# Optimization experiments

Measured on AMD Instinct MI355X. Metric: run time of the kernel, lower is better.

## Reference

```python
import jax, jax.numpy as jnp
import numpy as np

E = 8        # num_experts
K = 2        # num_experts_per_tok
H = 1024     # hidden_dim
F = 2816     # intermediate_dim
R = 256      # shared-core rank
B, S = 2, 1024


def setup_inputs() -> dict:
    key = jax.random.key(0)
    ks = jax.random.split(key, 12)
    inp = {
        "hidden_states": jax.random.normal(ks[0], (B, S, H), jnp.float32),
        "gate_w": jax.random.normal(ks[1], (H, E), jnp.float32) / np.sqrt(H),
        # gate_proj: hidden -> intermediate, factored W_e = Ug[e] @ Cg @ Vg[e]
        "Ug": jax.random.normal(ks[2], (E, H, R), jnp.float32) / np.sqrt(H),
        "Cg": jax.random.normal(ks[3], (R, R), jnp.float32) / np.sqrt(R),
        "Vg": jax.random.normal(ks[4], (E, R, F), jnp.float32) / np.sqrt(R),
        # up_proj: hidden -> intermediate
        "Uu": jax.random.normal(ks[5], (E, H, R), jnp.float32) / np.sqrt(H),
        "Cu": jax.random.normal(ks[6], (R, R), jnp.float32) / np.sqrt(R),
        "Vu": jax.random.normal(ks[7], (E, R, F), jnp.float32) / np.sqrt(R),
        # down_proj: intermediate -> hidden
        "Ud": jax.random.normal(ks[8], (E, F, R), jnp.float32) / np.sqrt(F),
        "Cd": jax.random.normal(ks[9], (R, R), jnp.float32) / np.sqrt(R),
        "Vd": jax.random.normal(ks[10], (E, R, H), jnp.float32) / np.sqrt(R),
    }
    return inp


def _moe_forward(x, gate_w, Ug, Cg, Vg, Uu, Cu, Vu, Ud, Cd, Vd):
    b, s, h = x.shape
    xf = x.reshape(-1, h)                       # [T, H]
    T = xf.shape[0]
    logits = xf @ gate_w                        # [T, E]
    probs = jax.nn.softmax(logits, axis=-1)
    w, idx = jax.lax.top_k(probs, K)            # [T, K]
    w = w / jnp.sum(w, axis=-1, keepdims=True)
    # dense combine weights: combine[t, e] = sum of renormalized routing
    # weights over top-k slots routed to expert e (scatter-add in torch code)
    combine = jnp.zeros((T, E), xf.dtype).at[jnp.arange(T)[:, None], idx].add(w)
    out = jnp.zeros_like(xf)
    for e in range(E):  # fixed small expert count
        g = (xf @ Ug[e]) @ Cg @ Vg[e]           # [T, F]
        u = (xf @ Uu[e]) @ Cu @ Vu[e]           # [T, F]
        a = jax.nn.silu(g) * u
        y = (a @ Ud[e]) @ Cd @ Vd[e]            # [T, H]
        out = out + combine[:, e:e + 1] * y
    return out.reshape(b, s, h)


def reference(hidden_states, gate_w, Ug, Cg, Vg, Uu, Cu, Vu, Ud, Cd, Vd):
    return _moe_forward(hidden_states, gate_w, Ug, Cg, Vg, Uu, Cu, Vu, Ud, Cd, Vd)
```

## Files before the change

kernel.cpp:

```cpp
#include <hip/hip_runtime.h>
#include <math.h>

constexpr int cE = 8;
constexpr int cH = 1024;
constexpr int cF = 2816;
constexpr int cR = 256;
constexpr int cT = 2048;
constexpr int ROWS = cT * 2;
constexpr int LDA = 40;

using short8  = __attribute__((ext_vector_type(8))) short;
using float4v = __attribute__((ext_vector_type(4))) float;
#define MFMA16 __builtin_amdgcn_mfma_f32_16x16x32_bf16

__device__ __forceinline__ unsigned short f2bf(float f) {
  union { float f; unsigned u; } v; v.f = f;
  unsigned r = v.u + 0x7fffu + ((v.u >> 16) & 1u);
  return (unsigned short)(r >> 16);
}
__device__ __forceinline__ float bf2f(unsigned short s) {
  union { unsigned u; float f; } v; v.u = (unsigned)s << 16; return v.f;
}

__device__ __forceinline__ void store_bf8(unsigned short* dst, float4 a, float4 b) {
  union { unsigned short u[8]; uint4 v; } t;
  t.u[0] = f2bf(a.x); t.u[1] = f2bf(a.y); t.u[2] = f2bf(a.z); t.u[3] = f2bf(a.w);
  t.u[4] = f2bf(b.x); t.u[5] = f2bf(b.y); t.u[6] = f2bf(b.z); t.u[7] = f2bf(b.w);
  *reinterpret_cast<uint4*>(dst) = t.v;
}

__device__ __forceinline__ void gld16(const unsigned short* g, unsigned short* l) {
  __builtin_amdgcn_global_load_lds(
      (const __attribute__((address_space(1))) void*)g,
      (__attribute__((address_space(3))) void*)l, 16, 0, 0);
}

__global__ __launch_bounds__(256) void k_gating(
    const float* __restrict__ x, const float* __restrict__ gw,
    unsigned short* __restrict__ xb, int* __restrict__ et,
    float* __restrict__ wt)
{
  const int tid = threadIdx.x;
  const int wid = tid >> 6, lane = tid & 63;
  const int t = blockIdx.x * 4 + wid;
  const float* xr = x + (long)t * cH + lane * 16;
  float4 v0 = *reinterpret_cast<const float4*>(xr);
  float4 v1 = *reinterpret_cast<const float4*>(xr + 4);
  float4 v2 = *reinterpret_cast<const float4*>(xr + 8);
  float4 v3 = *reinterpret_cast<const float4*>(xr + 12);
  store_bf8(xb + (long)t * cH + lane * 16, v0, v1);
  store_bf8(xb + (long)t * cH + lane * 16 + 8, v2, v3);
  float xv[16];
  *reinterpret_cast<float4*>(&xv[0])  = v0;
  *reinterpret_cast<float4*>(&xv[4])  = v1;
  *reinterpret_cast<float4*>(&xv[8])  = v2;
  *reinterpret_cast<float4*>(&xv[12]) = v3;
  const float* g = gw + (long)lane * 16 * cE;
  float l[cE];
#pragma unroll
  for (int e = 0; e < cE; ++e) l[e] = 0.f;
#pragma unroll
  for (int i = 0; i < 16; ++i) {
    float4 ga = *reinterpret_cast<const float4*>(g + i * cE);
    float4 gb = *reinterpret_cast<const float4*>(g + i * cE + 4);
    float xi = xv[i];
    l[0] += xi * ga.x; l[1] += xi * ga.y; l[2] += xi * ga.z; l[3] += xi * ga.w;
    l[4] += xi * gb.x; l[5] += xi * gb.y; l[6] += xi * gb.z; l[7] += xi * gb.w;
  }
#pragma unroll
  for (int m = 1; m < 64; m <<= 1)
#pragma unroll
    for (int e = 0; e < cE; ++e)
      l[e] += __shfl_xor(l[e], m, 64);
  if (lane == 0) {
    int i0 = 0; float m0 = l[0];
#pragma unroll
    for (int e = 1; e < cE; ++e) if (l[e] > m0) { m0 = l[e]; i0 = e; }
    int i1 = -1; float m1 = -1e30f;
#pragma unroll
    for (int e = 0; e < cE; ++e) if (e != i0 && l[e] > m1) { m1 = l[e]; i1 = e; }
    float w0 = 1.f / (1.f + expf(m1 - m0));
    et[t * 2 + 0] = i0;  et[t * 2 + 1] = i1;
    wt[t * 2 + 0] = w0;  wt[t * 2 + 1] = 1.f - w0;
  }
}

__global__ __launch_bounds__(256) void k_lists(
    const int* __restrict__ et, int* __restrict__ rowmap,
    int* __restrict__ tok, int* __restrict__ cnt, int* __restrict__ off)
{
  __shared__ int c[cE], p[cE], o[cE];
  const int tid = threadIdx.x;
  if (tid < cE) { c[tid] = 0; p[tid] = 0; }
  __syncthreads();
  for (int i = tid; i < ROWS; i += 256) atomicAdd(&c[et[i]], 1);
  __syncthreads();
  if (tid == 0) {
    int s = 0;
    for (int e = 0; e < cE; ++e) { o[e] = s; s += c[e]; }
  }
  __syncthreads();
  for (int i = tid; i < ROWS; i += 256) {
    int e = et[i];
    int slot = atomicAdd(&p[e], 1);
    int cr = o[e] + slot;
    rowmap[i] = cr;
    tok[cr] = i >> 1;
  }
  if (tid < cE) { cnt[tid] = c[tid]; off[tid] = o[tid]; }
}

__device__ __forceinline__ void tconv_tile(
    const float* __restrict__ in, unsigned short* __restrict__ out,
    int P, int Q, int e, int bx, int by, int tid, float (*tile)[33])
{
  const long es = (long)P * Q;
  in += e * es; out += e * es;
  const int c0 = bx * 32, r0 = by * 32;
  const int r = tid >> 3, c4 = (tid & 7) * 4;
  float4 v = *reinterpret_cast<const float4*>(in + (long)(r0 + r) * Q + c0 + c4);
  tile[r][c4 + 0] = v.x; tile[r][c4 + 1] = v.y;
  tile[r][c4 + 2] = v.z; tile[r][c4 + 3] = v.w;
  __syncthreads();
  const int cc = tid >> 3, rr4 = (tid & 7) * 4;
  ushort4 o;
  o.x = f2bf(tile[rr4 + 0][cc]);
  o.y = f2bf(tile[rr4 + 1][cc]);
  o.z = f2bf(tile[rr4 + 2][cc]);
  o.w = f2bf(tile[rr4 + 3][cc]);
  *reinterpret_cast<ushort4*>(out + (long)(c0 + cc) * P + r0 + rr4) = o;
}

constexpr int TCONV_BLOCKS = 19072;
__global__ __launch_bounds__(256) void k_tconv_all(
    const float* __restrict__ Cg, unsigned short* __restrict__ CgT,
    const float* __restrict__ Cu, unsigned short* __restrict__ CuT,
    const float* __restrict__ Vd, unsigned short* __restrict__ VdT,
    const float* __restrict__ Vg, unsigned short* __restrict__ vgT,
    const float* __restrict__ Vu, unsigned short* __restrict__ vuT,
    const float* __restrict__ Ud, unsigned short* __restrict__ udT)
{
  __shared__ float tile[32][33];
  int b = blockIdx.x;
  const float* in; unsigned short* out; int P, Q;
  if (b < 64)         { in = Cg; out = CgT; P = 256;  Q = 256;  }
  else if (b < 128)   { b -= 64;    in = Cu; out = CuT; P = 256;  Q = 256;  }
  else if (b < 2176)  { b -= 128;   in = Vd; out = VdT; P = 256;  Q = 1024; }
  else if (b < 7808)  { b -= 2176;  in = Vg; out = vgT; P = 256;  Q = 2816; }
  else if (b < 13440) { b -= 7808;  in = Vu; out = vuT; P = 256;  Q = 2816; }
  else                { b -= 13440; in = Ud; out = udT; P = 2816; Q = 256;  }
  const int tpe = (P / 32) * (Q / 32);
  const int e = b / tpe, rem = b % tpe;
  const int bx = rem % (Q / 32), by = rem / (Q / 32);
  tconv_tile(in, out, P, Q, e, bx, by, threadIdx.x, tile);
}

__device__ __forceinline__ void foldm_body(
    const unsigned short* __restrict__ A, const float* __restrict__ B,
    unsigned short* __restrict__ D, int ldd, int m0, int n0, int tid,
    unsigned short* As, unsigned short* Bs)
{
  const int sr = tid >> 2, sk = (tid & 3) * 8;
  const unsigned short* a0 = A + (long)(m0 + sr) * 256 + sk;
  const unsigned short* a1 = a0 + (long)64 * 256;
  const float* br = B + (long)(n0 + sr) * 256 + sk;
  uint4 rA0, rA1; float4 rB0, rB1;
  auto load_slice = [&](int k0) {
    rA0 = *reinterpret_cast<const uint4*>(a0 + k0);
    rA1 = *reinterpret_cast<const uint4*>(a1 + k0);
    rB0 = *reinterpret_cast<const float4*>(br + k0);
    rB1 = *reinterpret_cast<const float4*>(br + k0 + 4);
  };
  load_slice(0);
  const int wid = tid >> 6, lane = tid & 63;
  const int wm = (wid >> 1) * 64, wn = (wid & 1) * 32;
  const int fr = lane & 15, fq = lane >> 4;
  float4v zf = {0.f, 0.f, 0.f, 0.f};
  float4v acc[4][2];
#pragma unroll
  for (int i = 0; i < 4; ++i) { acc[i][0] = zf; acc[i][1] = zf; }
  for (int k0 = 0; k0 < 256; k0 += 32) {
    *reinterpret_cast<uint4*>(&As[sr * LDA + sk]) = rA0;
    *reinterpret_cast<uint4*>(&As[(sr + 64) * LDA + sk]) = rA1;
    store_bf8(&Bs[sr * LDA + sk], rB0, rB1);
    if (k0 + 32 < 256) load_slice(k0 + 32);
    __syncthreads();
    short8 af[4], bf[2];
#pragma unroll
    for (int mi = 0; mi < 4; ++mi)
      af[mi] = *reinterpret_cast<const short8*>(&As[(wm + mi * 16 + fr) * LDA + fq * 8]);
#pragma unroll
    for (int nj = 0; nj < 2; ++nj)
      bf[nj] = *reinterpret_cast<const short8*>(&Bs[(wn + nj * 16 + fr) * LDA + fq * 8]);
#pragma unroll
    for (int mi = 0; mi < 4; ++mi)
#pragma unroll
      for (int nj = 0; nj < 2; ++nj)
        acc[mi][nj] = MFMA16(af[mi], bf[nj], acc[mi][nj], 0, 0, 0);
    __syncthreads();
  }
#pragma unroll
  for (int mi = 0; mi < 4; ++mi)
#pragma unroll
    for (int r = 0; r < 4; ++r) {
      int m = m0 + wm + mi * 16 + fq * 4 + r;
#pragma unroll
      for (int nj = 0; nj < 2; ++nj)
        D[(long)m * ldd + n0 + wn + nj * 16 + fr] = f2bf(acc[mi][nj][r]);
    }
}

__global__ __launch_bounds__(256, 2) void k_foldm(
    const unsigned short* __restrict__ A, long sA,
    const float* __restrict__ B, long sB,
    unsigned short* __restrict__ D, long sD, int ldd)
{
  __shared__ __align__(16) unsigned short As[128 * LDA], Bs[64 * LDA];
  const int e = blockIdx.z;
  foldm_body(A + e * sA, B + e * sB, D + e * sD, ldd,
             blockIdx.y * 128, blockIdx.x * 64, threadIdx.x, As, Bs);
}

__global__ __launch_bounds__(256, 2) void k_foldm2(
    const unsigned short* __restrict__ A0, const unsigned short* __restrict__ A1,
    const float* __restrict__ B0, const float* __restrict__ B1,
    unsigned short* __restrict__ D)
{
  __shared__ __align__(16) unsigned short As[128 * LDA], Bs[64 * LDA];
  const int z = blockIdx.z, sel = z >> 3, e = z & 7;
  const unsigned short* A = sel ? A1 : A0;
  const float* B = (sel ? B1 : B0) + (long)e * cH * cR;
  unsigned short* Dp = D + (long)e * 512 * 1024 + (long)sel * 256 * 1024;
  foldm_body(A, B, Dp, cH, blockIdx.y * 128, blockIdx.x * 64, threadIdx.x, As, Bs);
}

__global__ __launch_bounds__(256, 2) void k_t1c(
    const unsigned short* __restrict__ xb, const unsigned short* __restrict__ b1t,
    unsigned short* __restrict__ t1, const int* __restrict__ tok,
    const int* __restrict__ cnt, const int* __restrict__ off)
{
  __shared__ __align__(16) unsigned short As[128 * 64], Bs[64 * 64];
  const int e = blockIdx.z, c = cnt[e], o = off[e];
  const int m0 = blockIdx.y * 128;
  if (m0 >= c) return;
  const int n0 = blockIdx.x * 64;
  const int tid = threadIdx.x;
  const int wid = tid >> 6, lane = tid & 63;
  const int sr8 = lane >> 3, sc = (lane & 7) * 8;
  const unsigned short* gA[4];
#pragma unroll
  for (int j = 0; j < 4; ++j) {
    int row = min(m0 + wid * 32 + j * 8 + sr8, c - 1);
    gA[j] = xb + (long)tok[o + row] * cH + sc;
  }
  const unsigned short* gB = b1t + (long)e * 512 * 1024 +
      (long)(n0 + wid * 16 + sr8) * 1024 + sc;
  unsigned short* lA = As + wid * 32 * 64;
  unsigned short* lB = Bs + wid * 16 * 64;
  const int wm = (wid >> 1) * 64, wn = (wid & 1) * 32;
  const int fr = lane & 15, fq = lane >> 4;
  float4v zf = {0.f, 0.f, 0.f, 0.f};
  float4v acc[4][2];
#pragma unroll
  for (int i = 0; i < 4; ++i) { acc[i][0] = zf; acc[i][1] = zf; }
  for (int k0 = 0; k0 < cH; k0 += 64) {
#pragma unroll
    for (int j = 0; j < 4; ++j) gld16(gA[j] + k0, lA + j * 8 * 64);
    gld16(gB + k0, lB);
    gld16(gB + (long)8 * 1024 + k0, lB + 8 * 64);
    __syncthreads();
#pragma unroll
    for (int ks = 0; ks < 2; ++ks) {
      short8 af[4], bf[2];
#pragma unroll
      for (int mi = 0; mi < 4; ++mi)
        af[mi] = *reinterpret_cast<const short8*>(
            &As[(wm + mi * 16 + fr) * 64 + ks * 32 + fq * 8]);
#pragma unroll
      for (int nj = 0; nj < 2; ++nj)
        bf[nj] = *reinterpret_cast<const short8*>(
            &Bs[(wn + nj * 16 + fr) * 64 + ks * 32 + fq * 8]);
#pragma unroll
      for (int mi = 0; mi < 4; ++mi)
#pragma unroll
        for (int nj = 0; nj < 2; ++nj)
          acc[mi][nj] = MFMA16(af[mi], bf[nj], acc[mi][nj], 0, 0, 0);
    }
    __syncthreads();
  }
#pragma unroll
  for (int mi = 0; mi < 4; ++mi)
#pragma unroll
    for (int r = 0; r < 4; ++r) {
      int row = m0 + wm + mi * 16 + fq * 4 + r;
      if (row < c) {
#pragma unroll
        for (int nj = 0; nj < 2; ++nj)
          t1[(long)(o + row) * 512 + n0 + wn + nj * 16 + fr] = f2bf(acc[mi][nj][r]);
      }
    }
}

__global__ __launch_bounds__(256, 2) void k_act(
    const unsigned short* __restrict__ t1,
    const unsigned short* __restrict__ vgT, const unsigned short* __restrict__ vuT,
    unsigned short* __restrict__ a, const int* __restrict__ cnt,
    const int* __restrict__ off)
{
  __shared__ __align__(16) unsigned short Ag[128 * 32], Au[128 * 32];
  __shared__ __align__(16) unsigned short Bg[64 * 32],  Bu[64 * 32];
  const int e = blockIdx.z, c = cnt[e], o = off[e];
  const int m0 = blockIdx.y * 128;
  if (m0 >= c) return;
  const int n0 = blockIdx.x * 64;
  const int tid = threadIdx.x;
  const int wid = tid >> 6, lane = tid & 63;
  const int sr16 = lane >> 2, sc = (lane & 3) * 8;
  const int ra0 = o + min(m0 + wid * 32 + sr16, c - 1);
  const int ra1 = o + min(m0 + wid * 32 + 16 + sr16, c - 1);
  const unsigned short* gAg0 = t1 + (long)ra0 * 512 + sc;
  const unsigned short* gAg1 = t1 + (long)ra1 * 512 + sc;
  const unsigned short* gBg = vgT + (long)e * cF * 256 + (long)(n0 + wid * 16 + sr16) * 256 + sc;
  const unsigned short* gBu = vuT + (long)e * cF * 256 + (long)(n0 + wid * 16 + sr16) * 256 + sc;
  unsigned short* lAg = Ag + wid * 32 * 32;
  unsigned short* lAu = Au + wid * 32 * 32;
  unsigned short* lBg = Bg + wid * 16 * 32;
  unsigned short* lBu = Bu + wid * 16 * 32;
  const int wm = (wid >> 1) * 64, wn = (wid & 1) * 32;
  const int fr = lane & 15, fq = lane >> 4;
  float4v zf = {0.f, 0.f, 0.f, 0.f};
  float4v accg[4][2], accu[4][2];
#pragma unroll
  for (int i = 0; i < 4; ++i) { accg[i][0] = zf; accg[i][1] = zf; accu[i][0] = zf; accu[i][1] = zf; }
  for (int k0 = 0; k0 < 256; k0 += 32) {
    gld16(gAg0 + k0, lAg);
    gld16(gAg1 + k0, lAg + 16 * 32);
    gld16(gAg0 + 256 + k0, lAu);
    gld16(gAg1 + 256 + k0, lAu + 16 * 32);
    gld16(gBg + k0, lBg);
    gld16(gBu + k0, lBu);
    __syncthreads();
    short8 ag[4], au[4], bg[2], bu[2];
#pragma unroll
    for (int mi = 0; mi < 4; ++mi) {
      ag[mi] = *reinterpret_cast<const short8*>(&Ag[(wm + mi * 16 + fr) * 32 + fq * 8]);
      au[mi] = *reinterpret_cast<const short8*>(&Au[(wm + mi * 16 + fr) * 32 + fq * 8]);
    }
#pragma unroll
    for (int nj = 0; nj < 2; ++nj) {
      bg[nj] = *reinterpret_cast<const short8*>(&Bg[(wn + nj * 16 + fr) * 32 + fq * 8]);
      bu[nj] = *reinterpret_cast<const short8*>(&Bu[(wn + nj * 16 + fr) * 32 + fq * 8]);
    }
#pragma unroll
    for (int mi = 0; mi < 4; ++mi)
#pragma unroll
      for (int nj = 0; nj < 2; ++nj) {
        accg[mi][nj] = MFMA16(ag[mi], bg[nj], accg[mi][nj], 0, 0, 0);
        accu[mi][nj] = MFMA16(au[mi], bu[nj], accu[mi][nj], 0, 0, 0);
      }
    __syncthreads();
  }
#pragma unroll
  for (int mi = 0; mi < 4; ++mi)
#pragma unroll
    for (int r = 0; r < 4; ++r) {
      int row = m0 + wm + mi * 16 + fq * 4 + r;
      if (row < c) {
#pragma unroll
        for (int nj = 0; nj < 2; ++nj) {
          float g = accg[mi][nj][r];
          float u = accu[mi][nj][r];
          float s = g / (1.f + expf(-g)) * u;
          a[(long)(o + row) * cF + n0 + wn + nj * 16 + fr] = f2bf(s);
        }
      }
    }
}

__global__ __launch_bounds__(256) void k_t3(
    const unsigned short* __restrict__ a, const unsigned short* __restrict__ udT,
    float* __restrict__ t3p, const int* __restrict__ cnt,
    const int* __restrict__ off)
{
  __shared__ __align__(16) unsigned short As[64 * 64], Bs[64 * 64];
  const int e = blockIdx.z, c = cnt[e], o = off[e];
  const int m0 = blockIdx.y * 64;
  if (m0 >= c) return;
  const int n0 = (blockIdx.x & 3) * 64;
  const int ksp = blockIdx.x >> 2;
  const int kbase = ksp * 704;
  const int tid = threadIdx.x;
  const int wid = tid >> 6, lane = tid & 63;
  const int sr8 = lane >> 3, sc = (lane & 7) * 8;
  const int ra0 = o + min(m0 + wid * 16 + sr8, c - 1);
  const int ra1 = o + min(m0 + wid * 16 + 8 + sr8, c - 1);
  const unsigned short* gA0 = a + (long)ra0 * cF + kbase + sc;
  const unsigned short* gA1 = a + (long)ra1 * cF + kbase + sc;
  const unsigned short* gB  = udT + (long)e * 256 * cF + (long)(n0 + wid * 16 + sr8) * cF + kbase + sc;
  unsigned short* lA = As + wid * 16 * 64;
  unsigned short* lB = Bs + wid * 16 * 64;
  const int wm = (wid >> 1) * 32, wn = (wid & 1) * 32;
  const int fr = lane & 15, fq = lane >> 4;
  float4v zf = {0.f, 0.f, 0.f, 0.f};
  float4v acc[2][2] = {{zf, zf}, {zf, zf}};
  for (int k0 = 0; k0 < 704; k0 += 64) {
    gld16(gA0 + k0, lA);
    gld16(gA1 + k0, lA + 8 * 64);
    gld16(gB + k0, lB);
    gld16(gB + (long)8 * cF + k0, lB + 8 * 64);
    __syncthreads();
#pragma unroll
    for (int ks = 0; ks < 2; ++ks) {
      short8 af[2], bf[2];
#pragma unroll
      for (int mi = 0; mi < 2; ++mi)
        af[mi] = *reinterpret_cast<const short8*>(
            &As[(wm + mi * 16 + fr) * 64 + ks * 32 + fq * 8]);
#pragma unroll
      for (int nj = 0; nj < 2; ++nj)
        bf[nj] = *reinterpret_cast<const short8*>(
            &Bs[(wn + nj * 16 + fr) * 64 + ks * 32 + fq * 8]);
#pragma unroll
      for (int mi = 0; mi < 2; ++mi)
#pragma unroll
        for (int nj = 0; nj < 2; ++nj)
          acc[mi][nj] = MFMA16(af[mi], bf[nj], acc[mi][nj], 0, 0, 0);
    }
    __syncthreads();
  }
  float* dstbase = t3p + (long)ksp * ROWS * 256;
#pragma unroll
  for (int mi = 0; mi < 2; ++mi)
#pragma unroll
    for (int r = 0; r < 4; ++r) {
      int row = m0 + wm + mi * 16 + fq * 4 + r;
      if (row < c) {
        float* dst = dstbase + (long)(o + row) * 256 + n0 + wn;
#pragma unroll
        for (int nj = 0; nj < 2; ++nj)
          dst[nj * 16 + fr] = acc[mi][nj][r];
      }
    }
}

__global__ __launch_bounds__(256) void k_red(
    const float* __restrict__ t3p, unsigned short* __restrict__ t3b)
{
  const long psz = (long)ROWS * 256;
  long i = ((long)blockIdx.x * 256 + threadIdx.x) * 8;
  float4 s0 = *reinterpret_cast<const float4*>(t3p + i);
  float4 s1 = *reinterpret_cast<const float4*>(t3p + i + 4);
#pragma unroll
  for (int q = 1; q < 4; ++q) {
    float4 a0 = *reinterpret_cast<const float4*>(t3p + q * psz + i);
    float4 a1 = *reinterpret_cast<const float4*>(t3p + q * psz + i + 4);
    s0.x += a0.x; s0.y += a0.y; s0.z += a0.z; s0.w += a0.w;
    s1.x += a1.x; s1.y += a1.y; s1.z += a1.z; s1.w += a1.w;
  }
  store_bf8(t3b + i, s0, s1);
}

__global__ __launch_bounds__(256, 2) void k_y(
    const unsigned short* __restrict__ t3b, const unsigned short* __restrict__ vd2t,
    unsigned short* __restrict__ y, const int* __restrict__ cnt,
    const int* __restrict__ off)
{
  __shared__ __align__(16) unsigned short As[128 * 32], Bs[64 * 32];
  const int e = blockIdx.z, c = cnt[e], o = off[e];
  const int m0 = blockIdx.y * 128;
  if (m0 >= c) return;
  const int n0 = blockIdx.x * 64;
  const int tid = threadIdx.x;
  const int wid = tid >> 6, lane = tid & 63;
  const int sr16 = lane >> 2, sc = (lane & 3) * 8;
  const int ra0 = o + min(m0 + wid * 32 + sr16, c - 1);
  const int ra1 = o + min(m0 + wid * 32 + 16 + sr16, c - 1);
  const unsigned short* gA0 = t3b + (long)ra0 * 256 + sc;
  const unsigned short* gA1 = t3b + (long)ra1 * 256 + sc;
  const unsigned short* gB  = vd2t + (long)e * cH * 256 + (long)(n0 + wid * 16 + sr16) * 256 + sc;
  unsigned short* lA = As + wid * 32 * 32;
  unsigned short* lB = Bs + wid * 16 * 32;
  const int wm = (wid >> 1) * 64, wn = (wid & 1) * 32;
  const int fr = lane & 15, fq = lane >> 4;
  float4v zf = {0.f, 0.f, 0.f, 0.f};
  float4v acc[4][2];
#pragma unroll
  for (int i = 0; i < 4; ++i) { acc[i][0] = zf; acc[i][1] = zf; }
  for (int k0 = 0; k0 < 256; k0 += 32) {
    gld16(gA0 + k0, lA);
    gld16(gA1 + k0, lA + 16 * 32);
    gld16(gB + k0, lB);
    __syncthreads();
    short8 af[4], bf[2];
#pragma unroll
    for (int mi = 0; mi < 4; ++mi)
      af[mi] = *reinterpret_cast<const short8*>(&As[(wm + mi * 16 + fr) * 32 + fq * 8]);
#pragma unroll
    for (int nj = 0; nj < 2; ++nj)
      bf[nj] = *reinterpret_cast<const short8*>(&Bs[(wn + nj * 16 + fr) * 32 + fq * 8]);
#pragma unroll
    for (int mi = 0; mi < 4; ++mi)
#pragma unroll
      for (int nj = 0; nj < 2; ++nj)
        acc[mi][nj] = MFMA16(af[mi], bf[nj], acc[mi][nj], 0, 0, 0);
    __syncthreads();
  }
#pragma unroll
  for (int mi = 0; mi < 4; ++mi)
#pragma unroll
    for (int r = 0; r < 4; ++r) {
      int row = m0 + wm + mi * 16 + fq * 4 + r;
      if (row < c) {
#pragma unroll
        for (int nj = 0; nj < 2; ++nj)
          y[(long)(o + row) * cH + n0 + wn + nj * 16 + fr] = f2bf(acc[mi][nj][r]);
      }
    }
}

__global__ __launch_bounds__(256) void k_combine(
    const unsigned short* __restrict__ y, const float* __restrict__ wt,
    const int* __restrict__ rowmap, float* __restrict__ out)
{
  const int tid = threadIdx.x;
  const int t = blockIdx.x * 2 + (tid >> 7);
  const int h = (tid & 127) * 8;
  const int r0 = rowmap[2 * t], r1 = rowmap[2 * t + 1];
  const float w0 = wt[2 * t], w1 = wt[2 * t + 1];
  union { uint4 v; unsigned short s[8]; } ua, ub;
  ua.v = *reinterpret_cast<const uint4*>(y + (long)r0 * cH + h);
  ub.v = *reinterpret_cast<const uint4*>(y + (long)r1 * cH + h);
  float o[8];
#pragma unroll
  for (int i = 0; i < 8; ++i)
    o[i] = w0 * bf2f(ua.s[i]) + w1 * bf2f(ub.s[i]);
  float* dst = out + (long)t * cH + h;
  *reinterpret_cast<float4*>(dst)     = make_float4(o[0], o[1], o[2], o[3]);
  *reinterpret_cast<float4*>(dst + 4) = make_float4(o[4], o[5], o[6], o[7]);
}

extern "C" void kernel_launch(void* const* d_in, const int* in_sizes, int n_in,
                              void* d_out, int out_size, void* d_ws, size_t ws_size,
                              hipStream_t stream)
{
  const float* x  = (const float*)d_in[0];
  const float* gw = (const float*)d_in[1];
  const float* Ug = (const float*)d_in[2];
  const float* Cg = (const float*)d_in[3];
  const float* Vg = (const float*)d_in[4];
  const float* Uu = (const float*)d_in[5];
  const float* Cu = (const float*)d_in[6];
  const float* Vu = (const float*)d_in[7];
  const float* Ud = (const float*)d_in[8];
  const float* Cd = (const float*)d_in[9];
  const float* Vd = (const float*)d_in[10];
  float* out = (float*)d_out;

  char* w = (char*)d_ws;
  unsigned short* vgT = (unsigned short*)w;
  float*          t3p = (float*)w;
  unsigned short* t3b = (unsigned short*)(w + (long)4 * ROWS * 256 * 4);
  w += (long)cE * cF * 256 * 2;
  unsigned short* b1t = (unsigned short*)w;  w += (long)cE * 512 * 1024 * 2;
  unsigned short* vd2t = (unsigned short*)w; w += (long)cE * cH * 256 * 2;
  unsigned short* vuT = (unsigned short*)w;
  unsigned short* yb  = (unsigned short*)w;  w += (long)cE * cF * 256 * 2;
  unsigned short* udT = (unsigned short*)w;  w += (long)cE * 256 * cF * 2;
  unsigned short* VdT = (unsigned short*)w;
  unsigned short* xb  = (unsigned short*)w;  w += (long)cE * cH * 256 * 2;
  unsigned short* CgT = (unsigned short*)w;  w += (long)cR * cR * 2;
  unsigned short* CuT = (unsigned short*)w;  w += (long)cR * cR * 2;
  unsigned short* t1  = (unsigned short*)w;  w += (long)ROWS * 512 * 2;
  unsigned short* ab  = (unsigned short*)w;  w += (long)ROWS * cF * 2;
  float* wt   = (float*)w; w += ROWS * 4;
  int* et     = (int*)w; w += ROWS * 4;
  int* rowmap = (int*)w; w += ROWS * 4;
  int* tok    = (int*)w; w += ROWS * 4;
  int* cnt = (int*)w; w += cE * 4;
  int* off = (int*)w; w += cE * 4;

  k_tconv_all<<<dim3(TCONV_BLOCKS), dim3(256), 0, stream>>>(
      Cg, CgT, Cu, CuT, Vd, VdT, Vg, vgT, Vu, vuT, Ud, udT);
  k_foldm2<<<dim3(cH / 64, cR / 128, 16), dim3(256), 0, stream>>>(
      CgT, CuT, Ug, Uu, b1t);
  k_foldm<<<dim3(cR / 64, cH / 128, cE), dim3(256), 0, stream>>>(
      VdT, (long)cH * cR, Cd, 0, vd2t, (long)cH * 256, cR);
  k_gating<<<dim3(cT / 4), dim3(256), 0, stream>>>(x, gw, xb, et, wt);
  k_lists<<<dim3(1), dim3(256), 0, stream>>>(et, rowmap, tok, cnt, off);
  k_t1c<<<dim3(8, cT / 128, cE), dim3(256), 0, stream>>>(xb, b1t, t1, tok, cnt, off);
  k_act<<<dim3(cF / 64, cT / 128, cE), dim3(256), 0, stream>>>(t1, vgT, vuT, ab, cnt, off);
  k_t3<<<dim3(16, cT / 64, cE), dim3(256), 0, stream>>>(ab, udT, t3p, cnt, off);
  k_red<<<dim3(ROWS * 256 / (256 * 8)), dim3(256), 0, stream>>>(t3p, t3b);
  k_y<<<dim3(cH / 64, cT / 128, cE), dim3(256), 0, stream>>>(t3b, vd2t, yb, cnt, off);
  k_combine<<<dim3(cT / 2), dim3(256), 0, stream>>>(yb, wt, rowmap, out);
}
```

Baseline: 293.0 us.

## Merge prep kernels into two launches and drop split-K in t3

Weight transpose/convert and gating are combined into one launch, and the foldm GEMMs and routing-list construction are combined into a second launch, cutting the launch count from five to two. k_t3 no longer splits K four ways into fp32 partials followed by a separate reduction kernel. It now runs the full K loop per block and writes bf16 directly, which removes the k_red launch and the partial-sum traffic. The cost is four times fewer t3 blocks, each with a longer serial K loop, which may reduce parallelism, and the workspace layout is adjusted to match.

```diff
diff --git a/kernel.cpp b/kernel.cpp
--- a/kernel.cpp
+++ b/kernel.cpp
@@ -35,80 +35,8 @@
       (__attribute__((address_space(3))) void*)l, 16, 0, 0);
 }
 
-__global__ __launch_bounds__(256) void k_gating(
-    const float* __restrict__ x, const float* __restrict__ gw,
-    unsigned short* __restrict__ xb, int* __restrict__ et,
-    float* __restrict__ wt)
-{
-  const int tid = threadIdx.x;
-  const int wid = tid >> 6, lane = tid & 63;
-  const int t = blockIdx.x * 4 + wid;
-  const float* xr = x + (long)t * cH + lane * 16;
-  float4 v0 = *reinterpret_cast<const float4*>(xr);
-  float4 v1 = *reinterpret_cast<const float4*>(xr + 4);
-  float4 v2 = *reinterpret_cast<const float4*>(xr + 8);
-  float4 v3 = *reinterpret_cast<const float4*>(xr + 12);
-  store_bf8(xb + (long)t * cH + lane * 16, v0, v1);
-  store_bf8(xb + (long)t * cH + lane * 16 + 8, v2, v3);
-  float xv[16];
-  *reinterpret_cast<float4*>(&xv[0])  = v0;
-  *reinterpret_cast<float4*>(&xv[4])  = v1;
-  *reinterpret_cast<float4*>(&xv[8])  = v2;
-  *reinterpret_cast<float4*>(&xv[12]) = v3;
-  const float* g = gw + (long)lane * 16 * cE;
-  float l[cE];
-#pragma unroll
-  for (int e = 0; e < cE; ++e) l[e] = 0.f;
-#pragma unroll
-  for (int i = 0; i < 16; ++i) {
-    float4 ga = *reinterpret_cast<const float4*>(g + i * cE);
-    float4 gb = *reinterpret_cast<const float4*>(g + i * cE + 4);
-    float xi = xv[i];
-    l[0] += xi * ga.x; l[1] += xi * ga.y; l[2] += xi * ga.z; l[3] += xi * ga.w;
-    l[4] += xi * gb.x; l[5] += xi * gb.y; l[6] += xi * gb.z; l[7] += xi * gb.w;
-  }
-#pragma unroll
-  for (int m = 1; m < 64; m <<= 1)
-#pragma unroll
-    for (int e = 0; e < cE; ++e)
-      l[e] += __shfl_xor(l[e], m, 64);
-  if (lane == 0) {
-    int i0 = 0; float m0 = l[0];
-#pragma unroll
-    for (int e = 1; e < cE; ++e) if (l[e] > m0) { m0 = l[e]; i0 = e; }
-    int i1 = -1; float m1 = -1e30f;
-#pragma unroll
-    for (int e = 0; e < cE; ++e) if (e != i0 && l[e] > m1) { m1 = l[e]; i1 = e; }
-    float w0 = 1.f / (1.f + expf(m1 - m0));
-    et[t * 2 + 0] = i0;  et[t * 2 + 1] = i1;
-    wt[t * 2 + 0] = w0;  wt[t * 2 + 1] = 1.f - w0;
-  }
-}
-
-__global__ __launch_bounds__(256) void k_lists(
-    const int* __restrict__ et, int* __restrict__ rowmap,
-    int* __restrict__ tok, int* __restrict__ cnt, int* __restrict__ off)
-{
-  __shared__ int c[cE], p[cE], o[cE];
-  const int tid = threadIdx.x;
-  if (tid < cE) { c[tid] = 0; p[tid] = 0; }
-  __syncthreads();
-  for (int i = tid; i < ROWS; i += 256) atomicAdd(&c[et[i]], 1);
-  __syncthreads();
-  if (tid == 0) {
-    int s = 0;
-    for (int e = 0; e < cE; ++e) { o[e] = s; s += c[e]; }
-  }
-  __syncthreads();
-  for (int i = tid; i < ROWS; i += 256) {
-    int e = et[i];
-    int slot = atomicAdd(&p[e], 1);
-    int cr = o[e] + slot;
-    rowmap[i] = cr;
-    tok[cr] = i >> 1;
-  }
-  if (tid < cE) { cnt[tid] = c[tid]; off[tid] = o[tid]; }
-}
+constexpr int TCONV_BLOCKS = 19072;
+constexpr int PREP1_BLOCKS = TCONV_BLOCKS + cT / 4;
 
 __device__ __forceinline__ void tconv_tile(
     const float* __restrict__ in, unsigned short* __restrict__ out,
@@ -131,28 +59,76 @@
   *reinterpret_cast<ushort4*>(out + (long)(c0 + cc) * P + r0 + rr4) = o;
 }
 
-constexpr int TCONV_BLOCKS = 19072;
-__global__ __launch_bounds__(256) void k_tconv_all(
+__global__ __launch_bounds__(256) void k_prep1(
     const float* __restrict__ Cg, unsigned short* __restrict__ CgT,
     const float* __restrict__ Cu, unsigned short* __restrict__ CuT,
     const float* __restrict__ Vd, unsigned short* __restrict__ VdT,
     const float* __restrict__ Vg, unsigned short* __restrict__ vgT,
     const float* __restrict__ Vu, unsigned short* __restrict__ vuT,
-    const float* __restrict__ Ud, unsigned short* __restrict__ udT)
+    const float* __restrict__ Ud, unsigned short* __restrict__ udT,
+    const float* __restrict__ x, const float* __restrict__ gw,
+    unsigned short* __restrict__ xb, int* __restrict__ et,
+    float* __restrict__ wt)
 {
   __shared__ float tile[32][33];
   int b = blockIdx.x;
-  const float* in; unsigned short* out; int P, Q;
-  if (b < 64)         { in = Cg; out = CgT; P = 256;  Q = 256;  }
-  else if (b < 128)   { b -= 64;    in = Cu; out = CuT; P = 256;  Q = 256;  }
-  else if (b < 2176)  { b -= 128;   in = Vd; out = VdT; P = 256;  Q = 1024; }
-  else if (b < 7808)  { b -= 2176;  in = Vg; out = vgT; P = 256;  Q = 2816; }
-  else if (b < 13440) { b -= 7808;  in = Vu; out = vuT; P = 256;  Q = 2816; }
-  else                { b -= 13440; in = Ud; out = udT; P = 2816; Q = 256;  }
-  const int tpe = (P / 32) * (Q / 32);
-  const int e = b / tpe, rem = b % tpe;
-  const int bx = rem % (Q / 32), by = rem / (Q / 32);
-  tconv_tile(in, out, P, Q, e, bx, by, threadIdx.x, tile);
+  const int tid = threadIdx.x;
+  if (b < TCONV_BLOCKS) {
+    const float* in; unsigned short* out; int P, Q;
+    if (b < 64)         { in = Cg; out = CgT; P = 256;  Q = 256;  }
+    else if (b < 128)   { b -= 64;    in = Cu; out = CuT; P = 256;  Q = 256;  }
+    else if (b < 2176)  { b -= 128;   in = Vd; out = VdT; P = 256;  Q = 1024; }
+    else if (b < 7808)  { b -= 2176;  in = Vg; out = vgT; P = 256;  Q = 2816; }
+    else if (b < 13440) { b -= 7808;  in = Vu; out = vuT; P = 256;  Q = 2816; }
+    else                { b -= 13440; in = Ud; out = udT; P = 2816; Q = 256;  }
+    const int tpe = (P / 32) * (Q / 32);
+    const int e = b / tpe, rem = b % tpe;
+    const int bx = rem % (Q / 32), by = rem / (Q / 32);
+    tconv_tile(in, out, P, Q, e, bx, by, tid, tile);
+    return;
+  }
+  const int wid = tid >> 6, lane = tid & 63;
+  const int t = (b - TCONV_BLOCKS) * 4 + wid;
+  const float* xr = x + (long)t * cH + lane * 16;
+  float4 v0 = *reinterpret_cast<const float4*>(xr);
+  float4 v1 = *reinterpret_cast<const float4*>(xr + 4);
+  float4 v2 = *reinterpret_cast<const float4*>(xr + 8);
+  float4 v3 = *reinterpret_cast<const float4*>(xr + 12);
+  store_bf8(xb + (long)t * cH + lane * 16, v0, v1);
+  store_bf8(xb + (long)t * cH + lane * 16 + 8, v2, v3);
+  float xv[16];
+  *reinterpret_cast<float4*>(&xv[0])  = v0;
+  *reinterpret_cast<float4*>(&xv[4])  = v1;
+  *reinterpret_cast<float4*>(&xv[8])  = v2;
+  *reinterpret_cast<float4*>(&xv[12]) = v3;
+  const float* g = gw + (long)lane * 16 * cE;
+  float l[cE];
+#pragma unroll
+  for (int e = 0; e < cE; ++e) l[e] = 0.f;
+#pragma unroll
+  for (int i = 0; i < 16; ++i) {
+    float4 ga = *reinterpret_cast<const float4*>(g + i * cE);
+    float4 gb = *reinterpret_cast<const float4*>(g + i * cE + 4);
+    float xi = xv[i];
+    l[0] += xi * ga.x; l[1] += xi * ga.y; l[2] += xi * ga.z; l[3] += xi * ga.w;
+    l[4] += xi * gb.x; l[5] += xi * gb.y; l[6] += xi * gb.z; l[7] += xi * gb.w;
+  }
+#pragma unroll
+  for (int m = 1; m < 64; m <<= 1)
+#pragma unroll
+    for (int e = 0; e < cE; ++e)
+      l[e] += __shfl_xor(l[e], m, 64);
+  if (lane == 0) {
+    int i0 = 0; float m0 = l[0];
+#pragma unroll
+    for (int e = 1; e < cE; ++e) if (l[e] > m0) { m0 = l[e]; i0 = e; }
+    int i1 = -1; float m1 = -1e30f;
+#pragma unroll
+    for (int e = 0; e < cE; ++e) if (e != i0 && l[e] > m1) { m1 = l[e]; i1 = e; }
+    float w0 = 1.f / (1.f + expf(m1 - m0));
+    et[t * 2 + 0] = i0;  et[t * 2 + 1] = i1;
+    wt[t * 2 + 0] = w0;  wt[t * 2 + 1] = 1.f - w0;
+  }
 }
 
 __device__ __forceinline__ void foldm_body(
@@ -210,28 +186,51 @@
     }
 }
 
-__global__ __launch_bounds__(256, 2) void k_foldm(
-    const unsigned short* __restrict__ A, long sA,
-    const float* __restrict__ B, long sB,
-    unsigned short* __restrict__ D, long sD, int ldd)
+constexpr int PREP2_BLOCKS = 512 + 256 + 1;
+__global__ __launch_bounds__(256, 2) void k_prep2(
+    const unsigned short* __restrict__ CgT, const unsigned short* __restrict__ CuT,
+    const float* __restrict__ Ug, const float* __restrict__ Uu,
+    unsigned short* __restrict__ b1t,
+    const unsigned short* __restrict__ VdT, const float* __restrict__ Cd,
+    unsigned short* __restrict__ vd2t,
+    const int* __restrict__ et, int* __restrict__ rowmap,
+    int* __restrict__ tok, int* __restrict__ cnt, int* __restrict__ off)
 {
   __shared__ __align__(16) unsigned short As[128 * LDA], Bs[64 * LDA];
-  const int e = blockIdx.z;
-  foldm_body(A + e * sA, B + e * sB, D + e * sD, ldd,
-             blockIdx.y * 128, blockIdx.x * 64, threadIdx.x, As, Bs);
-}
-
-__global__ __launch_bounds__(256, 2) void k_foldm2(
-    const unsigned short* __restrict__ A0, const unsigned short* __restrict__ A1,
-    const float* __restrict__ B0, const float* __restrict__ B1,
-    unsigned short* __restrict__ D)
-{
-  __shared__ __align__(16) unsigned short As[128 * LDA], Bs[64 * LDA];
-  const int z = blockIdx.z, sel = z >> 3, e = z & 7;
-  const unsigned short* A = sel ? A1 : A0;
-  const float* B = (sel ? B1 : B0) + (long)e * cH * cR;
-  unsigned short* Dp = D + (long)e * 512 * 1024 + (long)sel * 256 * 1024;
-  foldm_body(A, B, Dp, cH, blockIdx.y * 128, blockIdx.x * 64, threadIdx.x, As, Bs);
+  __shared__ int sc_[cE], sp_[cE], so_[cE];
+  const int b = blockIdx.x;
+  const int tid = threadIdx.x;
+  if (b < 512) {
+    const int bx = b & 15, by = (b >> 4) & 1, z = b >> 5;
+    const int sel = z >> 3, e = z & 7;
+    const unsigned short* A = sel ? CuT : CgT;
+    const float* B = (sel ? Uu : Ug) + (long)e * cH * cR;
+    unsigned short* Dp = b1t + (long)e * 512 * 1024 + (long)sel * 256 * 1024;
+    foldm_body(A, B, Dp, cH, by * 128, bx * 64, tid, As, Bs);
+  } else if (b < 768) {
+    const int b2 = b - 512;
+    const int bx = b2 & 3, by = (b2 >> 2) & 7, e = b2 >> 5;
+    foldm_body(VdT + (long)e * cH * cR, Cd, vd2t + (long)e * cH * 256, cR,
+               by * 128, bx * 64, tid, As, Bs);
+  } else {
+    if (tid < cE) { sc_[tid] = 0; sp_[tid] = 0; }
+    __syncthreads();
+    for (int i = tid; i < ROWS; i += 256) atomicAdd(&sc_[et[i]], 1);
+    __syncthreads();
+    if (tid == 0) {
+      int s = 0;
+      for (int e = 0; e < cE; ++e) { so_[e] = s; s += sc_[e]; }
+    }
+    __syncthreads();
+    for (int i = tid; i < ROWS; i += 256) {
+      int e = et[i];
+      int slot = atomicAdd(&sp_[e], 1);
+      int cr = so_[e] + slot;
+      rowmap[i] = cr;
+      tok[cr] = i >> 1;
+    }
+    if (tid < cE) { cnt[tid] = sc_[tid]; off[tid] = so_[tid]; }
+  }
 }
 
 __global__ __launch_bounds__(256, 2) void k_t1c(
@@ -377,33 +376,31 @@
     }
 }
 
-__global__ __launch_bounds__(256) void k_t3(
+__global__ __launch_bounds__(256, 2) void k_t3(
     const unsigned short* __restrict__ a, const unsigned short* __restrict__ udT,
-    float* __restrict__ t3p, const int* __restrict__ cnt,
+    unsigned short* __restrict__ t3b, const int* __restrict__ cnt,
     const int* __restrict__ off)
 {
   __shared__ __align__(16) unsigned short As[64 * 64], Bs[64 * 64];
   const int e = blockIdx.z, c = cnt[e], o = off[e];
   const int m0 = blockIdx.y * 64;
   if (m0 >= c) return;
-  const int n0 = (blockIdx.x & 3) * 64;
-  const int ksp = blockIdx.x >> 2;
-  const int kbase = ksp * 704;
+  const int n0 = blockIdx.x * 64;
   const int tid = threadIdx.x;
   const int wid = tid >> 6, lane = tid & 63;
   const int sr8 = lane >> 3, sc = (lane & 7) * 8;
   const int ra0 = o + min(m0 + wid * 16 + sr8, c - 1);
   const int ra1 = o + min(m0 + wid * 16 + 8 + sr8, c - 1);
-  const unsigned short* gA0 = a + (long)ra0 * cF + kbase + sc;
-  const unsigned short* gA1 = a + (long)ra1 * cF + kbase + sc;
-  const unsigned short* gB  = udT + (long)e * 256 * cF + (long)(n0 + wid * 16 + sr8) * cF + kbase + sc;
+  const unsigned short* gA0 = a + (long)ra0 * cF + sc;
+  const unsigned short* gA1 = a + (long)ra1 * cF + sc;
+  const unsigned short* gB  = udT + (long)e * 256 * cF + (long)(n0 + wid * 16 + sr8) * cF + sc;
   unsigned short* lA = As + wid * 16 * 64;
   unsigned short* lB = Bs + wid * 16 * 64;
   const int wm = (wid >> 1) * 32, wn = (wid & 1) * 32;
   const int fr = lane & 15, fq = lane >> 4;
   float4v zf = {0.f, 0.f, 0.f, 0.f};
   float4v acc[2][2] = {{zf, zf}, {zf, zf}};
-  for (int k0 = 0; k0 < 704; k0 += 64) {
+  for (int k0 = 0; k0 < cF; k0 += 64) {
     gld16(gA0 + k0, lA);
     gld16(gA1 + k0, lA + 8 * 64);
     gld16(gB + k0, lB);
@@ -428,36 +425,18 @@
     }
     __syncthreads();
   }
-  float* dstbase = t3p + (long)ksp * ROWS * 256;
 #pragma unroll
   for (int mi = 0; mi < 2; ++mi)
 #pragma unroll
     for (int r = 0; r < 4; ++r) {
       int row = m0 + wm + mi * 16 + fq * 4 + r;
       if (row < c) {
-        float* dst = dstbase + (long)(o + row) * 256 + n0 + wn;
+        unsigned short* dst = t3b + (long)(o + row) * 256 + n0 + wn;
 #pragma unroll
         for (int nj = 0; nj < 2; ++nj)
-          dst[nj * 16 + fr] = acc[mi][nj][r];
+          dst[nj * 16 + fr] = f2bf(acc[mi][nj][r]);
       }
     }
-}
-
-__global__ __launch_bounds__(256) void k_red(
-    const float* __restrict__ t3p, unsigned short* __restrict__ t3b)
-{
-  const long psz = (long)ROWS * 256;
-  long i = ((long)blockIdx.x * 256 + threadIdx.x) * 8;
-  float4 s0 = *reinterpret_cast<const float4*>(t3p + i);
-  float4 s1 = *reinterpret_cast<const float4*>(t3p + i + 4);
-#pragma unroll
-  for (int q = 1; q < 4; ++q) {
-    float4 a0 = *reinterpret_cast<const float4*>(t3p + q * psz + i);
-    float4 a1 = *reinterpret_cast<const float4*>(t3p + q * psz + i + 4);
-    s0.x += a0.x; s0.y += a0.y; s0.z += a0.z; s0.w += a0.w;
-    s1.x += a1.x; s1.y += a1.y; s1.z += a1.z; s1.w += a1.w;
-  }
-  store_bf8(t3b + i, s0, s1);
 }
 
 __global__ __launch_bounds__(256, 2) void k_y(
@@ -558,16 +537,15 @@
 
   char* w = (char*)d_ws;
   unsigned short* vgT = (unsigned short*)w;
-  float*          t3p = (float*)w;
-  unsigned short* t3b = (unsigned short*)(w + (long)4 * ROWS * 256 * 4);
+  unsigned short* t3b = (unsigned short*)w;
   w += (long)cE * cF * 256 * 2;
   unsigned short* b1t = (unsigned short*)w;  w += (long)cE * 512 * 1024 * 2;
   unsigned short* vd2t = (unsigned short*)w; w += (long)cE * cH * 256 * 2;
   unsigned short* vuT = (unsigned short*)w;
   unsigned short* yb  = (unsigned short*)w;  w += (long)cE * cF * 256 * 2;
   unsigned short* udT = (unsigned short*)w;  w += (long)cE * 256 * cF * 2;
-  unsigned short* VdT = (unsigned short*)w;
-  unsigned short* xb  = (unsigned short*)w;  w += (long)cE * cH * 256 * 2;
+  unsigned short* VdT = (unsigned short*)w;  w += (long)cE * cH * 256 * 2;
+  unsigned short* xb  = (unsigned short*)w;  w += (long)cT * cH * 2;
   unsigned short* CgT = (unsigned short*)w;  w += (long)cR * cR * 2;
   unsigned short* CuT = (unsigned short*)w;  w += (long)cR * cR * 2;
   unsigned short* t1  = (unsigned short*)w;  w += (long)ROWS * 512 * 2;
@@ -579,18 +557,13 @@
   int* cnt = (int*)w; w += cE * 4;
   int* off = (int*)w; w += cE * 4;
 
-  k_tconv_all<<<dim3(TCONV_BLOCKS), dim3(256), 0, stream>>>(
-      Cg, CgT, Cu, CuT, Vd, VdT, Vg, vgT, Vu, vuT, Ud, udT);
-  k_foldm2<<<dim3(cH / 64, cR / 128, 16), dim3(256), 0, stream>>>(
-      CgT, CuT, Ug, Uu, b1t);
-  k_foldm<<<dim3(cR / 64, cH / 128, cE), dim3(256), 0, stream>>>(
-      VdT, (long)cH * cR, Cd, 0, vd2t, (long)cH * 256, cR);
-  k_gating<<<dim3(cT / 4), dim3(256), 0, stream>>>(x, gw, xb, et, wt);
-  k_lists<<<dim3(1), dim3(256), 0, stream>>>(et, rowmap, tok, cnt, off);
+  k_prep1<<<dim3(PREP1_BLOCKS), dim3(256), 0, stream>>>(
+      Cg, CgT, Cu, CuT, Vd, VdT, Vg, vgT, Vu, vuT, Ud, udT, x, gw, xb, et, wt);
+  k_prep2<<<dim3(PREP2_BLOCKS), dim3(256), 0, stream>>>(
+      CgT, CuT, Ug, Uu, b1t, VdT, Cd, vd2t, et, rowmap, tok, cnt, off);
   k_t1c<<<dim3(8, cT / 128, cE), dim3(256), 0, stream>>>(xb, b1t, t1, tok, cnt, off);
   k_act<<<dim3(cF / 64, cT / 128, cE), dim3(256), 0, stream>>>(t1, vgT, vuT, ab, cnt, off);
-  k_t3<<<dim3(16, cT / 64, cE), dim3(256), 0, stream>>>(ab, udT, t3p, cnt, off);
-  k_red<<<dim3(ROWS * 256 / (256 * 8)), dim3(256), 0, stream>>>(t3p, t3b);
+  k_t3<<<dim3(4, cT / 64, cE), dim3(256), 0, stream>>>(ab, udT, t3b, cnt, off);
   k_y<<<dim3(cH / 64, cT / 128, cE), dim3(256), 0, stream>>>(t3b, vd2t, yb, cnt, off);
   k_combine<<<dim3(cT / 2), dim3(256), 0, stream>>>(yb, wt, rowmap, out);
 }
```

New measurement: 308.1 us. 1.05x slower.
